# Kernel tuning notes

Hardware: AMD Instinct MI355X
Metric: run time of the kernel (lower is better)

The kernel has to match this reference:

```python
import jax, jax.numpy as jnp
import numpy as np

B = 32768
IN_DIM = 1024
HID = 64
COMM = 256          # comm_dim == proto_latent_dim (num_simultaneous_tokens=1)
K = 8192            # num_protos
BETA = 0.25
KL_WEIGHT = 1.0


def setup_inputs() -> dict:
    key = jax.random.key(0)
    ks = jax.random.split(key, 16)
    def lin(kw, fan_in, shape):
        bound = 1.0 / np.sqrt(fan_in)
        return jax.random.uniform(kw, shape, jnp.float32, -bound, bound)
    return {
        "x": jax.random.normal(ks[0], (B, IN_DIM), jnp.float32),
        "eps": jax.random.normal(ks[1], (B, COMM), jnp.float32),
        "W_feat": lin(ks[2], IN_DIM, (IN_DIM, HID)),
        "b_feat": lin(ks[3], IN_DIM, (HID,)),
        "W0": lin(ks[4], HID, (HID, HID)),
        "b0": lin(ks[5], HID, (HID,)),
        "W1": lin(ks[6], HID, (HID, COMM)),
        "b1": lin(ks[7], HID, (COMM,)),
        "W_mu": lin(ks[8], COMM, (COMM, COMM)),
        "b_mu": lin(ks[9], COMM, (COMM,)),
        "W_var": lin(ks[10], COMM, (COMM, COMM)),
        "b_var": lin(ks[11], COMM, (COMM,)),
        "protos": jax.random.uniform(ks[12], (K, COMM), jnp.float32, -1.0 / K, 1.0 / K),
    }


def reference(x, eps, W_feat, b_feat, W0, b0, W1, b1, W_mu, b_mu, W_var, b_var, protos):
    # feature embedder + MLP (num_layers=2, relu after each)
    h = x @ W_feat + b_feat                       # [B, 64]
    h = jax.nn.relu(h @ W0 + b0)                  # [B, 64]
    h = jax.nn.relu(h @ W1 + b1)                  # [B, 256]
    # variational head
    mu = h @ W_mu + b_mu                          # [B, 256]
    logvar = h @ W_var + b_var                    # [B, 256]
    sample = mu + eps * jnp.exp(0.5 * logvar)     # reparameterize
    # VQ layer: pairwise sq-distances to codebook, argmin, gather
    d = (jnp.sum(sample * sample, axis=1, keepdims=True)
         + jnp.sum(protos * protos, axis=1)
         - 2.0 * (sample @ protos.T))             # [B, K]
    idx = jnp.argmin(d, axis=1)                   # [B]
    q = jnp.take(protos, idx, axis=0)             # [B, 256] == one_hot @ protos
    commitment = jnp.mean((jax.lax.stop_gradient(q) - sample) ** 2)
    embedding = jnp.mean((q - jax.lax.stop_gradient(sample)) ** 2)
    vq_loss = BETA * commitment + embedding
    q_st = sample + jax.lax.stop_gradient(q - sample)  # straight-through
    # KL to standard normal
    kld = jnp.mean(-0.5 * jnp.sum(1.0 + logvar - mu * mu - jnp.exp(logvar), axis=1))
    total_loss = KL_WEIGHT * kld + vq_loss
    return q_st, total_loss, kld
```

## Files before the change

kernel.cpp:

```cpp
#include <hip/hip_runtime.h>
#include <cfloat>

#define B_SZ   32768
#define IN_D   1024
#define HID    64
#define COMM   256
#define NPROTO 8192

#define SSCALE 12.0f
#define PSCALE 1.0e6f

typedef __attribute__((ext_vector_type(8))) short bf16x8;
typedef __attribute__((ext_vector_type(4))) float f32x4;
typedef __attribute__((ext_vector_type(4))) int   i32x4;

#define AS1 __attribute__((address_space(1)))
#define AS3 __attribute__((address_space(3)))

__device__ __forceinline__ unsigned short f2bf(float f) {
    unsigned u = __float_as_uint(f);
    unsigned r = u + 0x7fff + ((u >> 16) & 1);
    return (unsigned short)(r >> 16);
}

__device__ __forceinline__ int f2i8(float f, float scale) {
    float v = fminf(fmaxf(f * scale, -127.f), 127.f);
    return __float2int_rn(v);
}

__global__ __launch_bounds__(256) void prep_weights(
    const float* __restrict__ Wf,  const float* __restrict__ W0,
    const float* __restrict__ W1,  const float* __restrict__ Wmu,
    const float* __restrict__ Wvar,
    unsigned short* __restrict__ Wft, unsigned short* __restrict__ W0t,
    unsigned short* __restrict__ W1t, unsigned short* __restrict__ Wmt,
    unsigned short* __restrict__ Wvt)
{
    int gid = blockIdx.x * 256 + threadIdx.x;
    const float* src; unsigned short* dst; int off, K, N;
    if (gid < 65536)       { src = Wf;  dst = Wft; off = gid;          K = 1024; N = 64;  }
    else if (gid < 69632)  { src = W0;  dst = W0t; off = gid - 65536;  K = 64;   N = 64;  }
    else if (gid < 86016)  { src = W1;  dst = W1t; off = gid - 69632;  K = 64;   N = 256; }
    else if (gid < 151552) { src = Wmu; dst = Wmt; off = gid - 86016;  K = 256;  N = 256; }
    else                   { src = Wvar;dst = Wvt; off = gid - 151552; K = 256;  N = 256; }
    int k = off / N, n = off % N;
    dst[(size_t)n * K + k] = f2bf(src[off]);
}

__global__ __launch_bounds__(256) void pnorm_conv_kernel(const float* __restrict__ protos,
                                                         float* __restrict__ pnormS,
                                                         char* __restrict__ protoq)
{
    int g    = blockIdx.x * 256 + threadIdx.x;
    int p    = g >> 6;
    int lane = g & 63;
    float4 v = *(const float4*)&protos[(size_t)p * COMM + lane * 4];
    int b0 = f2i8(v.x, PSCALE) & 0xff;
    int b1 = f2i8(v.y, PSCALE) & 0xff;
    int b2 = f2i8(v.z, PSCALE) & 0xff;
    int b3 = f2i8(v.w, PSCALE) & 0xff;
    int pk = b0 | (b1 << 8) | (b2 << 16) | (b3 << 24);
    int T = p >> 7, jc = lane >> 2;
    *(int*)(protoq + ((size_t)(T * 16 + jc) * 128 + (p & 127)) * 16 + (lane & 3) * 4) = pk;
    float s = v.x * v.x + v.y * v.y + v.z * v.z + v.w * v.w;
#pragma unroll
    for (int off = 32; off; off >>= 1) s += __shfl_down(s, off);
    if (lane == 0) pnormS[p] = s * (SSCALE * PSCALE);
}

__global__ __launch_bounds__(256) void mlp_fused(
    const float* __restrict__ x,
    const unsigned short* __restrict__ Wft, const float* __restrict__ b_feat,
    const unsigned short* __restrict__ W0t, const float* __restrict__ b0,
    const unsigned short* __restrict__ W1t, const float* __restrict__ b1,
    unsigned short* __restrict__ h3b)
{
    __shared__ __align__(16) char lds[65536];
    short* Xs  = (short*)lds;
    short* Ws  = (short*)(lds + 8192);
    short* H1  = (short*)(lds + 16384);
    short* H2  = (short*)(lds + 24576);
    short* W1s = (short*)(lds + 32768);

    const int t   = threadIdx.x;
    const int w   = t >> 6;
    const int l   = t & 63;
    const int q   = l >> 4;
    const int j16 = l & 15;
    const int rowBase = blockIdx.x * 64;
    const int m = 16 * w + j16;

    float4 xr[2][2];
    int   xp[2];
    auto loadX = [&](int ks) {
#pragma unroll
        for (int i = 0; i < 2; ++i) {
            int p  = i * 256 + t;
            int r  = p >> 3;
            int js = p & 7;
            int j  = js ^ (r & 7);
            const float4* g = (const float4*)(x + (size_t)(rowBase + r) * IN_D + ks * 64 + j * 8);
            xr[i][0] = g[0];
            xr[i][1] = g[1];
            xp[i] = p;
        }
    };

    f32x4 acc1[4];
#pragma unroll
    for (int v = 0; v < 4; ++v) acc1[v] = (f32x4){0.f, 0.f, 0.f, 0.f};

    loadX(0);
    for (int ks = 0; ks < 16; ++ks) {
        __syncthreads();
#pragma unroll
        for (int i = 0; i < 2; ++i) {
            bf16x8 o;
            o[0] = (short)f2bf(xr[i][0].x); o[1] = (short)f2bf(xr[i][0].y);
            o[2] = (short)f2bf(xr[i][0].z); o[3] = (short)f2bf(xr[i][0].w);
            o[4] = (short)f2bf(xr[i][1].x); o[5] = (short)f2bf(xr[i][1].y);
            o[6] = (short)f2bf(xr[i][1].z); o[7] = (short)f2bf(xr[i][1].w);
            *(bf16x8*)((char*)Xs + (size_t)xp[i] * 16) = o;
        }
#pragma unroll
        for (int i = 0; i < 2; ++i) {
            int p  = i * 256 + t;
            int r  = p >> 3;
            int js = p & 7;
            int j  = js ^ (r & 7);
            const unsigned short* gw = Wft + (size_t)r * IN_D + ks * 64 + j * 8;
            void* dw = (char*)Ws + (size_t)(i * 256 + w * 64) * 16;
            __builtin_amdgcn_global_load_lds(
                (const AS1 void*)gw, (AS3 void*)dw, 16, 0, 0);
        }
        if (ks < 15) loadX(ks + 1);
        __syncthreads();
#pragma unroll
        for (int kk = 0; kk < 2; ++kk) {
            int jw = kk * 4 + q;
            bf16x8 af = *(const bf16x8*)((char*)Xs + (size_t)(m * 8 + (jw ^ (m & 7))) * 16);
#pragma unroll
            for (int v = 0; v < 4; ++v) {
                int n = 16 * v + j16;
                bf16x8 bf = *(const bf16x8*)((char*)Ws + (size_t)(n * 8 + (jw ^ (n & 7))) * 16);
                acc1[v] = __builtin_amdgcn_mfma_f32_16x16x32_bf16(af, bf, acc1[v], 0, 0, 0);
            }
        }
    }
#pragma unroll
    for (int v = 0; v < 4; ++v) {
        int c = 16 * v + j16;
        float bb = b_feat[c];
#pragma unroll
        for (int rg = 0; rg < 4; ++rg) {
            int r = 16 * w + q * 4 + rg;
            float h = acc1[v][rg] + bb;
            *(short*)((char*)H1 + (size_t)(r * 8 + ((c >> 3) ^ (r & 7))) * 16 + (c & 7) * 2)
                = (short)f2bf(h);
        }
    }

    __syncthreads();
#pragma unroll
    for (int i = 0; i < 2; ++i) {
        int p  = i * 256 + t;
        int n  = p >> 3;
        int js = p & 7;
        int j  = js ^ (n & 7);
        const unsigned short* gw = W0t + (size_t)n * 64 + j * 8;
        void* dw = (char*)Ws + (size_t)(i * 256 + w * 64) * 16;
        __builtin_amdgcn_global_load_lds(
            (const AS1 void*)gw, (AS3 void*)dw, 16, 0, 0);
    }
    __syncthreads();
    f32x4 acc2[4];
#pragma unroll
    for (int v = 0; v < 4; ++v) acc2[v] = (f32x4){0.f, 0.f, 0.f, 0.f};
#pragma unroll
    for (int kk = 0; kk < 2; ++kk) {
        int jw = kk * 4 + q;
        bf16x8 af = *(const bf16x8*)((char*)H1 + (size_t)(m * 8 + (jw ^ (m & 7))) * 16);
#pragma unroll
        for (int v = 0; v < 4; ++v) {
            int n = 16 * v + j16;
            bf16x8 bf = *(const bf16x8*)((char*)Ws + (size_t)(n * 8 + (jw ^ (n & 7))) * 16);
            acc2[v] = __builtin_amdgcn_mfma_f32_16x16x32_bf16(af, bf, acc2[v], 0, 0, 0);
        }
    }
#pragma unroll
    for (int v = 0; v < 4; ++v) {
        int c = 16 * v + j16;
        float bb = b0[c];
#pragma unroll
        for (int rg = 0; rg < 4; ++rg) {
            int r = 16 * w + q * 4 + rg;
            float h = fmaxf(acc2[v][rg] + bb, 0.f);
            *(short*)((char*)H2 + (size_t)(r * 8 + ((c >> 3) ^ (r & 7))) * 16 + (c & 7) * 2)
                = (short)f2bf(h);
        }
    }

    __syncthreads();
#pragma unroll
    for (int i = 0; i < 8; ++i) {
        int p  = i * 256 + t;
        int n  = p >> 3;
        int js = p & 7;
        int j  = js ^ (n & 7);
        const unsigned short* gw = W1t + (size_t)n * 64 + j * 8;
        void* dw = (char*)W1s + (size_t)(i * 256 + w * 64) * 16;
        __builtin_amdgcn_global_load_lds(
            (const AS1 void*)gw, (AS3 void*)dw, 16, 0, 0);
    }
    __syncthreads();
    f32x4 acc3[16];
#pragma unroll
    for (int v = 0; v < 16; ++v) acc3[v] = (f32x4){0.f, 0.f, 0.f, 0.f};
#pragma unroll
    for (int kk = 0; kk < 2; ++kk) {
        int jw = kk * 4 + q;
        bf16x8 af = *(const bf16x8*)((char*)H2 + (size_t)(m * 8 + (jw ^ (m & 7))) * 16);
#pragma unroll
        for (int v = 0; v < 16; ++v) {
            int n = 16 * v + j16;
            bf16x8 bf = *(const bf16x8*)((char*)W1s + (size_t)(n * 8 + (jw ^ (n & 7))) * 16);
            acc3[v] = __builtin_amdgcn_mfma_f32_16x16x32_bf16(af, bf, acc3[v], 0, 0, 0);
        }
    }
#pragma unroll
    for (int v = 0; v < 16; ++v) {
        int c = 16 * v + j16;
        float bb = b1[c];
#pragma unroll
        for (int rg = 0; rg < 4; ++rg) {
            int row = rowBase + 16 * w + q * 4 + rg;
            float h = fmaxf(acc3[v][rg] + bb, 0.f);
            h3b[(size_t)row * COMM + c] = f2bf(h);
        }
    }
}

__global__ __launch_bounds__(256) void head_mfma(
    const unsigned short* __restrict__ h3b,
    const unsigned short* __restrict__ Wmt, const float* __restrict__ bmu,
    const unsigned short* __restrict__ Wvt, const float* __restrict__ bvar,
    const float* __restrict__ eps,
    float* __restrict__ sample,
    char* __restrict__ sampleq,
    float* __restrict__ klpart)
{
    __shared__ __align__(16) char lds[49152];
    short* H3 = (short*)lds;
    short* Wm = (short*)(lds + 32768);
    short* Wv = (short*)(lds + 40960);

    const int t   = threadIdx.x;
    const int w   = t >> 6;
    const int l   = t & 63;
    const int q   = l >> 4;
    const int j16 = l & 15;
    const int rowBase = blockIdx.x * 64;
    const int m = 16 * w + j16;

#pragma unroll
    for (int i = 0; i < 8; ++i) {
        int p  = i * 256 + t;
        int r  = p >> 5;
        int js = p & 31;
        int j  = (js & 24) | ((js & 7) ^ (r & 7));
        const unsigned short* g = h3b + (size_t)(rowBase + r) * COMM + j * 8;
        void* d = (char*)H3 + (size_t)(i * 256 + w * 64) * 16;
        __builtin_amdgcn_global_load_lds(
            (const AS1 void*)g, (AS3 void*)d, 16, 0, 0);
    }

    float kl = 0.f;
    for (int c = 0; c < 4; ++c) {
        f32x4 am[4], av[4];
#pragma unroll
        for (int v = 0; v < 4; ++v) {
            am[v] = (f32x4){0.f, 0.f, 0.f, 0.f};
            av[v] = (f32x4){0.f, 0.f, 0.f, 0.f};
        }
        for (int ks = 0; ks < 4; ++ks) {
            __syncthreads();
#pragma unroll
            for (int i = 0; i < 2; ++i) {
                int p  = i * 256 + t;
                int n  = p >> 3;
                int js = p & 7;
                int j  = js ^ (n & 7);
                const unsigned short* gm =
                    Wmt + (size_t)(c * 64 + n) * COMM + ks * 64 + j * 8;
                const unsigned short* gv =
                    Wvt + (size_t)(c * 64 + n) * COMM + ks * 64 + j * 8;
                void* dm = (char*)Wm + (size_t)(i * 256 + w * 64) * 16;
                void* dv = (char*)Wv + (size_t)(i * 256 + w * 64) * 16;
                __builtin_amdgcn_global_load_lds(
                    (const AS1 void*)gm, (AS3 void*)dm, 16, 0, 0);
                __builtin_amdgcn_global_load_lds(
                    (const AS1 void*)gv, (AS3 void*)dv, 16, 0, 0);
            }
            __syncthreads();
#pragma unroll
            for (int kk = 0; kk < 2; ++kk) {
                int jwg = ks * 8 + kk * 4 + q;
                bf16x8 af = *(const bf16x8*)((char*)H3 +
                    (size_t)(m * 32 + ((jwg & 24) | ((jwg & 7) ^ (m & 7)))) * 16);
                int jw = kk * 4 + q;
#pragma unroll
                for (int v = 0; v < 4; ++v) {
                    int n = 16 * v + j16;
                    size_t pos = (size_t)(n * 8 + (jw ^ (n & 7))) * 16;
                    bf16x8 bm = *(const bf16x8*)((char*)Wm + pos);
                    bf16x8 bv = *(const bf16x8*)((char*)Wv + pos);
                    am[v] = __builtin_amdgcn_mfma_f32_16x16x32_bf16(af, bm, am[v], 0, 0, 0);
                    av[v] = __builtin_amdgcn_mfma_f32_16x16x32_bf16(af, bv, av[v], 0, 0, 0);
                }
            }
        }
#pragma unroll
        for (int v = 0; v < 4; ++v) {
            int col = c * 64 + 16 * v + j16;
            float bm_ = bmu[col];
            float bv_ = bvar[col];
#pragma unroll
            for (int rg = 0; rg < 4; ++rg) {
                int row = rowBase + 16 * w + q * 4 + rg;
                float mu = am[v][rg] + bm_;
                float lv = av[v][rg] + bv_;
                float e  = expf(0.5f * lv);
                float s  = mu + eps[(size_t)row * COMM + col] * e;
                sample [(size_t)row * COMM + col] = s;
                sampleq[(size_t)row * COMM + col] = (char)f2i8(s, SSCALE);
                kl += 1.f + lv - mu * mu - e * e;
            }
        }
    }
#pragma unroll
    for (int off = 32; off; off >>= 1) kl += __shfl_down(kl, off);
    __shared__ float wsum[4];
    if (l == 0) wsum[w] = kl;
    __syncthreads();
    if (t == 0)
        klpart[blockIdx.x] = wsum[0] + wsum[1] + wsum[2] + wsum[3];
}

#define SPLITS 4
#define SPAN   (NPROTO / SPLITS)
#define NT     (SPAN / 128)

__global__ __launch_bounds__(256) void vq_argmin_i8(
    const char* __restrict__ sampleq,
    const char* __restrict__ protoq,
    const float* __restrict__ pnormS,
    float* __restrict__ minval,
    int* __restrict__ minidx)
{
    __shared__ __align__(16) char As[32768];
    __shared__ __align__(16) char Bs[2][8192];

    const int t   = threadIdx.x;
    const int w   = t >> 6;
    const int l   = t & 63;
    const int q   = l >> 4;
    const int j16 = l & 15;
    const int wrow = (w >> 1) * 64;
    const int wcol = (w & 1) * 64;
    const int rowBase = blockIdx.x * 128;
    const int tBase   = blockIdx.y * NT;

#pragma unroll
    for (int i = 0; i < 8; ++i) {
        int p  = i * 256 + t;
        int r  = p >> 4;
        int cs = p & 15;
        int j  = cs ^ (r & 15);
        const char* g = sampleq + (size_t)(rowBase + r) * COMM + j * 16;
        void* d = As + (size_t)(i * 256 + w * 64) * 16;
        __builtin_amdgcn_global_load_lds(
            (const AS1 void*)g, (AS3 void*)d, 16, 0, 0);
    }
    {
        const char* src = protoq + (size_t)tBase * 32768;
#pragma unroll
        for (int i = 0; i < 2; ++i) {
            int p = i * 256 + t;
            __builtin_amdgcn_global_load_lds(
                (const AS1 void*)(src + (size_t)p * 16),
                (AS3 void*)(Bs[0] + (size_t)(i * 256 + w * 64) * 16), 16, 0, 0);
        }
    }

    float bestv[16];
    int   besti[16];
#pragma unroll
    for (int s = 0; s < 16; ++s) { bestv[s] = FLT_MAX; besti[s] = 0; }

    int buf = 0;
    for (int pt = 0; pt < NT; ++pt) {
        i32x4 acc[4][4];
#pragma unroll
        for (int u = 0; u < 4; ++u)
#pragma unroll
            for (int v = 0; v < 4; ++v) acc[u][v] = (i32x4){0, 0, 0, 0};

        for (int ks = 0; ks < 4; ++ks) {
            __syncthreads();
            int nks = ks + 1, npt = pt;
            if (nks == 4) { nks = 0; ++npt; }
            if (npt < NT) {
                const char* src = protoq + ((size_t)(tBase + npt) * 16 + nks * 4) * 2048;
#pragma unroll
                for (int i = 0; i < 2; ++i) {
                    int p = i * 256 + t;
                    __builtin_amdgcn_global_load_lds(
                        (const AS1 void*)(src + (size_t)p * 16),
                        (AS3 void*)(Bs[buf ^ 1] + (size_t)(i * 256 + w * 64) * 16), 16, 0, 0);
                }
            }
            i32x4 af[4], bfv[4];
            int jc = ks * 4 + q;
#pragma unroll
            for (int u = 0; u < 4; ++u) {
                int mm = wrow + 16 * u + j16;
                af[u] = *(const i32x4*)(As + (size_t)(mm * 16 + (jc ^ (mm & 15))) * 16);
            }
#pragma unroll
            for (int v = 0; v < 4; ++v) {
                int n = wcol + 16 * v + j16;
                bfv[v] = *(const i32x4*)(Bs[buf] + (size_t)(q * 128 + n) * 16);
            }
#pragma unroll
            for (int u = 0; u < 4; ++u)
#pragma unroll
                for (int v = 0; v < 4; ++v)
                    acc[u][v] = __builtin_amdgcn_mfma_i32_16x16x64_i8(
                        af[u], bfv[v], acc[u][v], 0, 0, 0);
            buf ^= 1;
        }
        int pTile = (tBase + pt) * 128;
#pragma unroll
        for (int v = 0; v < 4; ++v) {
            int col  = pTile + wcol + 16 * v + j16;
            float pn = pnormS[col];
#pragma unroll
            for (int u = 0; u < 4; ++u)
#pragma unroll
                for (int rg = 0; rg < 4; ++rg) {
                    float sc   = pn - 2.f * (float)acc[u][v][rg];
                    int   slot = u * 4 + rg;
                    if (sc < bestv[slot]) { bestv[slot] = sc; besti[slot] = col; }
                }
        }
    }
#pragma unroll
    for (int off = 1; off < 16; off <<= 1) {
#pragma unroll
        for (int s = 0; s < 16; ++s) {
            float ov = __shfl_xor(bestv[s], off);
            int   oi = __shfl_xor(besti[s], off);
            if (ov < bestv[s] || (ov == bestv[s] && oi < besti[s])) {
                bestv[s] = ov; besti[s] = oi;
            }
        }
    }
    __syncthreads();
    float* cv = (float*)Bs;
    int*   ci = ((int*)Bs) + 256;
    if (j16 == 0) {
#pragma unroll
        for (int u = 0; u < 4; ++u)
#pragma unroll
            for (int rg = 0; rg < 4; ++rg) {
                int row = wrow + 16 * u + 4 * q + rg;
                cv[(w & 1) * 128 + row] = bestv[u * 4 + rg];
                ci[(w & 1) * 128 + row] = besti[u * 4 + rg];
            }
    }
    __syncthreads();
    if (t < 128) {
        float v0 = cv[t];       int i0 = ci[t];
        float v1 = cv[128 + t]; int i1 = ci[128 + t];
        if (v1 < v0 || (v1 == v0 && i1 < i0)) { v0 = v1; i0 = i1; }
        minval[(size_t)blockIdx.y * B_SZ + rowBase + t] = v0;
        minidx[(size_t)blockIdx.y * B_SZ + rowBase + t] = i0;
    }
}

__global__ __launch_bounds__(256) void gather_kernel(const float* __restrict__ sample,
                                                     const float* __restrict__ protos,
                                                     const float* __restrict__ minval,
                                                     const int* __restrict__ minidx,
                                                     float* __restrict__ out,
                                                     float* __restrict__ msepart)
{
    int t  = threadIdx.x;
    int rb = blockIdx.x * 8;
    __shared__ int sidx[8];
    if (t < 8) {
        int i = rb + t;
        float bv = minval[i];
        int   bi = minidx[i];
#pragma unroll
        for (int s = 1; s < SPLITS; ++s) {
            float v = minval[(size_t)s * B_SZ + i];
            int   j = minidx[(size_t)s * B_SZ + i];
            if (v < bv || (v == bv && j < bi)) { bv = v; bi = j; }
        }
        sidx[t] = bi;
    }
    __syncthreads();
    float part = 0.f;
#pragma unroll
    for (int u = 0; u < 8; ++u) {
        int i  = rb + u;
        int id = sidx[u];
        float qv = protos[(size_t)id * COMM + t];
        float s  = sample[(size_t)i * COMM + t];
        float d  = qv - s;
        out[(size_t)i * COMM + t] = s + d;
        part += d * d;
    }
#pragma unroll
    for (int off = 32; off; off >>= 1) part += __shfl_down(part, off);
    __shared__ float wsum[4];
    if ((t & 63) == 0) wsum[t >> 6] = part;
    __syncthreads();
    if (t == 0) msepart[blockIdx.x] = wsum[0] + wsum[1] + wsum[2] + wsum[3];
}

__global__ __launch_bounds__(256) void finalize_kernel(const float* __restrict__ klpart, int nkl,
                                                       const float* __restrict__ msepart, int nmse,
                                                       float* __restrict__ out)
{
    int t = threadIdx.x;
    double kl = 0.0, mse = 0.0;
    for (int i = t; i < nkl;  i += 256) kl  += (double)klpart[i];
    for (int i = t; i < nmse; i += 256) mse += (double)msepart[i];
#pragma unroll
    for (int off = 32; off; off >>= 1) {
        kl  += __shfl_down(kl, off);
        mse += __shfl_down(mse, off);
    }
    __shared__ double skl[4], smse[4];
    if ((t & 63) == 0) { skl[t >> 6] = kl; smse[t >> 6] = mse; }
    __syncthreads();
    if (t == 0) {
        double K  = skl[0] + skl[1] + skl[2] + skl[3];
        double M  = smse[0] + smse[1] + smse[2] + smse[3];
        double kld = -0.5 * K / (double)B_SZ;
        double vq  = 1.25 * M / ((double)B_SZ * (double)COMM);
        out[(size_t)B_SZ * COMM]     = (float)(kld + vq);
        out[(size_t)B_SZ * COMM + 1] = (float)kld;
    }
}

extern "C" void kernel_launch(void* const* d_in, const int* in_sizes, int n_in,
                              void* d_out, int out_size, void* d_ws, size_t ws_size,
                              hipStream_t stream)
{
    const float* x      = (const float*)d_in[0];
    const float* eps    = (const float*)d_in[1];
    const float* W_feat = (const float*)d_in[2];
    const float* b_feat = (const float*)d_in[3];
    const float* W0     = (const float*)d_in[4];
    const float* b0     = (const float*)d_in[5];
    const float* W1     = (const float*)d_in[6];
    const float* b1     = (const float*)d_in[7];
    const float* W_mu   = (const float*)d_in[8];
    const float* b_mu   = (const float*)d_in[9];
    const float* W_var  = (const float*)d_in[10];
    const float* b_var  = (const float*)d_in[11];
    const float* protos = (const float*)d_in[12];
    float* out = (float*)d_out;

    char* wsb = (char*)d_ws;
    size_t off = 0;
    auto alloc = [&](size_t bytes) -> void* {
        void* p = wsb + off;
        off = (off + bytes + 255) & ~(size_t)255;
        return p;
    };
    unsigned short* Wft     = (unsigned short*)alloc((size_t)IN_D * HID * 2);
    unsigned short* W0t     = (unsigned short*)alloc((size_t)HID * HID * 2);
    unsigned short* W1t     = (unsigned short*)alloc((size_t)HID * COMM * 2);
    unsigned short* Wmt     = (unsigned short*)alloc((size_t)COMM * COMM * 2);
    unsigned short* Wvt     = (unsigned short*)alloc((size_t)COMM * COMM * 2);
    unsigned short* h3b     = (unsigned short*)alloc((size_t)B_SZ * COMM * 2);
    float*          sample  = (float*)alloc((size_t)B_SZ * COMM * 4);
    char*           sampleq = (char*) alloc((size_t)B_SZ * COMM);
    char*           protoq  = (char*) alloc((size_t)NPROTO * COMM);
    float*          pnormS  = (float*)alloc((size_t)NPROTO * 4);
    float*          minval  = (float*)alloc((size_t)SPLITS * B_SZ * 4);
    int*            minidx  = (int*)  alloc((size_t)SPLITS * B_SZ * 4);
    float*          klpart  = (float*)alloc(512 * 4);
    float*          msepart = (float*)alloc(4096 * 4);

    prep_weights<<<848, 256, 0, stream>>>(W_feat, W0, W1, W_mu, W_var,
                                          Wft, W0t, W1t, Wmt, Wvt);
    pnorm_conv_kernel<<<NPROTO / 4, 256, 0, stream>>>(protos, pnormS, protoq);
    mlp_fused<<<B_SZ / 64, 256, 0, stream>>>(x, Wft, b_feat, W0t, b0, W1t, b1, h3b);
    head_mfma<<<B_SZ / 64, 256, 0, stream>>>(h3b, Wmt, b_mu, Wvt, b_var, eps,
                                             sample, sampleq, klpart);
    vq_argmin_i8<<<dim3(B_SZ / 128, SPLITS), 256, 0, stream>>>(sampleq, protoq, pnormS,
                                                               minval, minidx);
    gather_kernel<<<B_SZ / 8, 256, 0, stream>>>(sample, protos, minval, minidx,
                                                out, msepart);
    finalize_kernel<<<1, 256, 0, stream>>>(klpart, 512, msepart, 4096, out);
}
```

Baseline: 428.6 us.

## Merge prep kernels, halve MLP/head row tiles, double-buffer MLP, hoist VQ A-fragments

The two preprocessing kernels are merged into one launch. The MLP and head kernels now use 32-row blocks with a 2x2 wave split, smaller LDS footprints and occupancy hints. The MLP now stages fp32 x straight into LDS with async loads, double-buffers it, and converts to bf16 at fragment load time. The VQ argmin kernel loads all A fragments into registers once instead of on every k-step, and skips the first barrier. The cost is more blocks, duplicated W loads per block, and higher register pressure in the VQ kernel.

```diff
diff --git a/kernel.cpp b/kernel.cpp
--- a/kernel.cpp
+++ b/kernel.cpp
@@ -28,219 +28,217 @@
     return __float2int_rn(v);
 }
 
-__global__ __launch_bounds__(256) void prep_weights(
+__global__ __launch_bounds__(256) void prep_all(
     const float* __restrict__ Wf,  const float* __restrict__ W0,
     const float* __restrict__ W1,  const float* __restrict__ Wmu,
-    const float* __restrict__ Wvar,
+    const float* __restrict__ Wvar, const float* __restrict__ protos,
     unsigned short* __restrict__ Wft, unsigned short* __restrict__ W0t,
     unsigned short* __restrict__ W1t, unsigned short* __restrict__ Wmt,
-    unsigned short* __restrict__ Wvt)
+    unsigned short* __restrict__ Wvt,
+    float* __restrict__ pnormS, char* __restrict__ protoq)
 {
-    int gid = blockIdx.x * 256 + threadIdx.x;
-    const float* src; unsigned short* dst; int off, K, N;
-    if (gid < 65536)       { src = Wf;  dst = Wft; off = gid;          K = 1024; N = 64;  }
-    else if (gid < 69632)  { src = W0;  dst = W0t; off = gid - 65536;  K = 64;   N = 64;  }
-    else if (gid < 86016)  { src = W1;  dst = W1t; off = gid - 69632;  K = 64;   N = 256; }
-    else if (gid < 151552) { src = Wmu; dst = Wmt; off = gid - 86016;  K = 256;  N = 256; }
-    else                   { src = Wvar;dst = Wvt; off = gid - 151552; K = 256;  N = 256; }
-    int k = off / N, n = off % N;
-    dst[(size_t)n * K + k] = f2bf(src[off]);
-}
-
-__global__ __launch_bounds__(256) void pnorm_conv_kernel(const float* __restrict__ protos,
-                                                         float* __restrict__ pnormS,
-                                                         char* __restrict__ protoq)
-{
-    int g    = blockIdx.x * 256 + threadIdx.x;
-    int p    = g >> 6;
-    int lane = g & 63;
-    float4 v = *(const float4*)&protos[(size_t)p * COMM + lane * 4];
-    int b0 = f2i8(v.x, PSCALE) & 0xff;
-    int b1 = f2i8(v.y, PSCALE) & 0xff;
-    int b2 = f2i8(v.z, PSCALE) & 0xff;
-    int b3 = f2i8(v.w, PSCALE) & 0xff;
-    int pk = b0 | (b1 << 8) | (b2 << 16) | (b3 << 24);
-    int T = p >> 7, jc = lane >> 2;
-    *(int*)(protoq + ((size_t)(T * 16 + jc) * 128 + (p & 127)) * 16 + (lane & 3) * 4) = pk;
-    float s = v.x * v.x + v.y * v.y + v.z * v.z + v.w * v.w;
-#pragma unroll
-    for (int off = 32; off; off >>= 1) s += __shfl_down(s, off);
-    if (lane == 0) pnormS[p] = s * (SSCALE * PSCALE);
-}
-
-__global__ __launch_bounds__(256) void mlp_fused(
+    int bid = blockIdx.x;
+    if (bid < 848) {
+        int gid = bid * 256 + threadIdx.x;
+        const float* src; unsigned short* dst; int off, K, N;
+        if (gid < 65536)       { src = Wf;  dst = Wft; off = gid;          K = 1024; N = 64;  }
+        else if (gid < 69632)  { src = W0;  dst = W0t; off = gid - 65536;  K = 64;   N = 64;  }
+        else if (gid < 86016)  { src = W1;  dst = W1t; off = gid - 69632;  K = 64;   N = 256; }
+        else if (gid < 151552) { src = Wmu; dst = Wmt; off = gid - 86016;  K = 256;  N = 256; }
+        else                   { src = Wvar;dst = Wvt; off = gid - 151552; K = 256;  N = 256; }
+        int k = off / N, n = off % N;
+        dst[(size_t)n * K + k] = f2bf(src[off]);
+    } else {
+        int g    = (bid - 848) * 256 + threadIdx.x;
+        int p    = g >> 6;
+        int lane = g & 63;
+        float4 v = *(const float4*)&protos[(size_t)p * COMM + lane * 4];
+        int b0 = f2i8(v.x, PSCALE) & 0xff;
+        int b1 = f2i8(v.y, PSCALE) & 0xff;
+        int b2 = f2i8(v.z, PSCALE) & 0xff;
+        int b3 = f2i8(v.w, PSCALE) & 0xff;
+        int pk = b0 | (b1 << 8) | (b2 << 16) | (b3 << 24);
+        int T = p >> 7, jc = lane >> 2;
+        *(int*)(protoq + ((size_t)(T * 16 + jc) * 128 + (p & 127)) * 16 + (lane & 3) * 4) = pk;
+        float s = v.x * v.x + v.y * v.y + v.z * v.z + v.w * v.w;
+#pragma unroll
+        for (int off = 32; off; off >>= 1) s += __shfl_down(s, off);
+        if (lane == 0) pnormS[p] = s * (SSCALE * PSCALE);
+    }
+}
+
+__global__ __launch_bounds__(256, 4) void mlp_fused(
     const float* __restrict__ x,
     const unsigned short* __restrict__ Wft, const float* __restrict__ b_feat,
     const unsigned short* __restrict__ W0t, const float* __restrict__ b0,
     const unsigned short* __restrict__ W1t, const float* __restrict__ b1,
     unsigned short* __restrict__ h3b)
 {
-    __shared__ __align__(16) char lds[65536];
-    short* Xs  = (short*)lds;
-    short* Ws  = (short*)(lds + 8192);
-    short* H1  = (short*)(lds + 16384);
-    short* H2  = (short*)(lds + 24576);
-    short* W1s = (short*)(lds + 32768);
+    __shared__ __align__(16) char lds[40960];
+    char* Xs0 = lds;
+    char* Xs1 = lds + 8192;
+    char* Ws0 = lds + 16384;
+    char* Ws1 = lds + 24576;
+    char* H1  = lds + 32768;
+    char* H2  = lds + 36864;
 
     const int t   = threadIdx.x;
     const int w   = t >> 6;
     const int l   = t & 63;
     const int q   = l >> 4;
     const int j16 = l & 15;
-    const int rowBase = blockIdx.x * 64;
-    const int m = 16 * w + j16;
-
-    float4 xr[2][2];
-    int   xp[2];
-    auto loadX = [&](int ks) {
+    const int rh  = w >> 1;
+    const int ch  = w & 1;
+    const int rowBase = blockIdx.x * 32;
+    const int m = rh * 16 + j16;
+
+    auto stageX = [&](int ks, char* dst) {
 #pragma unroll
         for (int i = 0; i < 2; ++i) {
             int p  = i * 256 + t;
-            int r  = p >> 3;
-            int js = p & 7;
-            int j  = js ^ (r & 7);
-            const float4* g = (const float4*)(x + (size_t)(rowBase + r) * IN_D + ks * 64 + j * 8);
-            xr[i][0] = g[0];
-            xr[i][1] = g[1];
-            xp[i] = p;
+            int r  = p >> 4;
+            int cs = p & 15;
+            int j  = cs ^ (r & 15);
+            const float* g = x + (size_t)(rowBase + r) * IN_D + ks * 64 + j * 4;
+            void* d = dst + (size_t)(i * 256 + w * 64) * 16;
+            __builtin_amdgcn_global_load_lds((const AS1 void*)g, (AS3 void*)d, 16, 0, 0);
         }
     };
-
-    f32x4 acc1[4];
-#pragma unroll
-    for (int v = 0; v < 4; ++v) acc1[v] = (f32x4){0.f, 0.f, 0.f, 0.f};
-
-    loadX(0);
-    for (int ks = 0; ks < 16; ++ks) {
-        __syncthreads();
-#pragma unroll
-        for (int i = 0; i < 2; ++i) {
-            bf16x8 o;
-            o[0] = (short)f2bf(xr[i][0].x); o[1] = (short)f2bf(xr[i][0].y);
-            o[2] = (short)f2bf(xr[i][0].z); o[3] = (short)f2bf(xr[i][0].w);
-            o[4] = (short)f2bf(xr[i][1].x); o[5] = (short)f2bf(xr[i][1].y);
-            o[6] = (short)f2bf(xr[i][1].z); o[7] = (short)f2bf(xr[i][1].w);
-            *(bf16x8*)((char*)Xs + (size_t)xp[i] * 16) = o;
-        }
+    auto stageW = [&](const unsigned short* Wt, int ldk, int ks, char* dst) {
 #pragma unroll
         for (int i = 0; i < 2; ++i) {
             int p  = i * 256 + t;
-            int r  = p >> 3;
-            int js = p & 7;
-            int j  = js ^ (r & 7);
-            const unsigned short* gw = Wft + (size_t)r * IN_D + ks * 64 + j * 8;
-            void* dw = (char*)Ws + (size_t)(i * 256 + w * 64) * 16;
-            __builtin_amdgcn_global_load_lds(
-                (const AS1 void*)gw, (AS3 void*)dw, 16, 0, 0);
-        }
-        if (ks < 15) loadX(ks + 1);
+            int n  = p >> 3;
+            int cs = p & 7;
+            int j  = cs ^ (n & 7);
+            const unsigned short* g = Wt + (size_t)n * ldk + ks * 64 + j * 8;
+            void* d = dst + (size_t)(i * 256 + w * 64) * 16;
+            __builtin_amdgcn_global_load_lds((const AS1 void*)g, (AS3 void*)d, 16, 0, 0);
+        }
+    };
+    auto afragX = [&](const char* Xsb, int kk) -> bf16x8 {
+        int jc = kk * 8 + q * 2;
+        f32x4 a0 = *(const f32x4*)(Xsb + (size_t)(m * 16 + (jc ^ (m & 15))) * 16);
+        f32x4 a1 = *(const f32x4*)(Xsb + (size_t)(m * 16 + ((jc + 1) ^ (m & 15))) * 16);
+        bf16x8 o;
+        o[0] = (short)f2bf(a0[0]); o[1] = (short)f2bf(a0[1]);
+        o[2] = (short)f2bf(a0[2]); o[3] = (short)f2bf(a0[3]);
+        o[4] = (short)f2bf(a1[0]); o[5] = (short)f2bf(a1[1]);
+        o[6] = (short)f2bf(a1[2]); o[7] = (short)f2bf(a1[3]);
+        return o;
+    };
+    auto bfrag = [&](const char* Wsb, int kk, int v) -> bf16x8 {
+        int n  = ch * 32 + 16 * v + j16;
+        int jc = kk * 4 + q;
+        return *(const bf16x8*)(Wsb + (size_t)(n * 8 + (jc ^ (n & 7))) * 16);
+    };
+    auto afragH = [&](const char* Hs, int kk) -> bf16x8 {
+        int jc = kk * 4 + q;
+        return *(const bf16x8*)(Hs + (size_t)(m * 8 + (jc ^ (m & 7))) * 16);
+    };
+
+    f32x4 acc1[2];
+#pragma unroll
+    for (int v = 0; v < 2; ++v) acc1[v] = (f32x4){0.f, 0.f, 0.f, 0.f};
+
+    stageX(0, Xs0);
+    stageW(Wft, IN_D, 0, Ws0);
+    for (int ks = 0; ks < 16; ++ks) {
+        int buf = ks & 1;
         __syncthreads();
+        if (ks < 15) {
+            stageX(ks + 1, buf ? Xs0 : Xs1);
+            stageW(Wft, IN_D, ks + 1, buf ? Ws0 : Ws1);
+        }
+        const char* Xsb = buf ? Xs1 : Xs0;
+        const char* Wsb = buf ? Ws1 : Ws0;
 #pragma unroll
         for (int kk = 0; kk < 2; ++kk) {
-            int jw = kk * 4 + q;
-            bf16x8 af = *(const bf16x8*)((char*)Xs + (size_t)(m * 8 + (jw ^ (m & 7))) * 16);
-#pragma unroll
-            for (int v = 0; v < 4; ++v) {
-                int n = 16 * v + j16;
-                bf16x8 bf = *(const bf16x8*)((char*)Ws + (size_t)(n * 8 + (jw ^ (n & 7))) * 16);
-                acc1[v] = __builtin_amdgcn_mfma_f32_16x16x32_bf16(af, bf, acc1[v], 0, 0, 0);
-            }
-        }
-    }
-#pragma unroll
-    for (int v = 0; v < 4; ++v) {
-        int c = 16 * v + j16;
+            bf16x8 af = afragX(Xsb, kk);
+#pragma unroll
+            for (int v = 0; v < 2; ++v)
+                acc1[v] = __builtin_amdgcn_mfma_f32_16x16x32_bf16(
+                    af, bfrag(Wsb, kk, v), acc1[v], 0, 0, 0);
+        }
+    }
+#pragma unroll
+    for (int v = 0; v < 2; ++v) {
+        int c = ch * 32 + 16 * v + j16;
         float bb = b_feat[c];
 #pragma unroll
         for (int rg = 0; rg < 4; ++rg) {
-            int r = 16 * w + q * 4 + rg;
+            int r = rh * 16 + q * 4 + rg;
             float h = acc1[v][rg] + bb;
-            *(short*)((char*)H1 + (size_t)(r * 8 + ((c >> 3) ^ (r & 7))) * 16 + (c & 7) * 2)
+            *(short*)(H1 + (size_t)(r * 8 + ((c >> 3) ^ (r & 7))) * 16 + (c & 7) * 2)
                 = (short)f2bf(h);
         }
     }
-
-    __syncthreads();
-#pragma unroll
-    for (int i = 0; i < 2; ++i) {
-        int p  = i * 256 + t;
-        int n  = p >> 3;
-        int js = p & 7;
-        int j  = js ^ (n & 7);
-        const unsigned short* gw = W0t + (size_t)n * 64 + j * 8;
-        void* dw = (char*)Ws + (size_t)(i * 256 + w * 64) * 16;
-        __builtin_amdgcn_global_load_lds(
-            (const AS1 void*)gw, (AS3 void*)dw, 16, 0, 0);
-    }
-    __syncthreads();
-    f32x4 acc2[4];
-#pragma unroll
-    for (int v = 0; v < 4; ++v) acc2[v] = (f32x4){0.f, 0.f, 0.f, 0.f};
+    stageW(W0t, 64, 0, Ws0);
+    __syncthreads();
+
+    f32x4 acc2[2];
+#pragma unroll
+    for (int v = 0; v < 2; ++v) acc2[v] = (f32x4){0.f, 0.f, 0.f, 0.f};
 #pragma unroll
     for (int kk = 0; kk < 2; ++kk) {
-        int jw = kk * 4 + q;
-        bf16x8 af = *(const bf16x8*)((char*)H1 + (size_t)(m * 8 + (jw ^ (m & 7))) * 16);
-#pragma unroll
-        for (int v = 0; v < 4; ++v) {
-            int n = 16 * v + j16;
-            bf16x8 bf = *(const bf16x8*)((char*)Ws + (size_t)(n * 8 + (jw ^ (n & 7))) * 16);
-            acc2[v] = __builtin_amdgcn_mfma_f32_16x16x32_bf16(af, bf, acc2[v], 0, 0, 0);
-        }
-    }
-#pragma unroll
-    for (int v = 0; v < 4; ++v) {
-        int c = 16 * v + j16;
+        bf16x8 af = afragH(H1, kk);
+#pragma unroll
+        for (int v = 0; v < 2; ++v)
+            acc2[v] = __builtin_amdgcn_mfma_f32_16x16x32_bf16(
+                af, bfrag(Ws0, kk, v), acc2[v], 0, 0, 0);
+    }
+#pragma unroll
+    for (int v = 0; v < 2; ++v) {
+        int c = ch * 32 + 16 * v + j16;
         float bb = b0[c];
 #pragma unroll
         for (int rg = 0; rg < 4; ++rg) {
-            int r = 16 * w + q * 4 + rg;
+            int r = rh * 16 + q * 4 + rg;
             float h = fmaxf(acc2[v][rg] + bb, 0.f);
-            *(short*)((char*)H2 + (size_t)(r * 8 + ((c >> 3) ^ (r & 7))) * 16 + (c & 7) * 2)
+            *(short*)(H2 + (size_t)(r * 8 + ((c >> 3) ^ (r & 7))) * 16 + (c & 7) * 2)
                 = (short)f2bf(h);
         }
     }
-
-    __syncthreads();
-#pragma unroll
-    for (int i = 0; i < 8; ++i) {
-        int p  = i * 256 + t;
-        int n  = p >> 3;
-        int js = p & 7;
-        int j  = js ^ (n & 7);
-        const unsigned short* gw = W1t + (size_t)n * 64 + j * 8;
-        void* dw = (char*)W1s + (size_t)(i * 256 + w * 64) * 16;
-        __builtin_amdgcn_global_load_lds(
-            (const AS1 void*)gw, (AS3 void*)dw, 16, 0, 0);
-    }
-    __syncthreads();
-    f32x4 acc3[16];
-#pragma unroll
-    for (int v = 0; v < 16; ++v) acc3[v] = (f32x4){0.f, 0.f, 0.f, 0.f};
-#pragma unroll
-    for (int kk = 0; kk < 2; ++kk) {
-        int jw = kk * 4 + q;
-        bf16x8 af = *(const bf16x8*)((char*)H2 + (size_t)(m * 8 + (jw ^ (m & 7))) * 16);
-#pragma unroll
-        for (int v = 0; v < 16; ++v) {
-            int n = 16 * v + j16;
-            bf16x8 bf = *(const bf16x8*)((char*)W1s + (size_t)(n * 8 + (jw ^ (n & 7))) * 16);
-            acc3[v] = __builtin_amdgcn_mfma_f32_16x16x32_bf16(af, bf, acc3[v], 0, 0, 0);
-        }
-    }
-#pragma unroll
-    for (int v = 0; v < 16; ++v) {
-        int c = 16 * v + j16;
-        float bb = b1[c];
-#pragma unroll
-        for (int rg = 0; rg < 4; ++rg) {
-            int row = rowBase + 16 * w + q * 4 + rg;
-            float h = fmaxf(acc3[v][rg] + bb, 0.f);
-            h3b[(size_t)row * COMM + c] = f2bf(h);
-        }
-    }
-}
-
-__global__ __launch_bounds__(256) void head_mfma(
+    stageW(W1t, 64, 0, Ws1);
+    __syncthreads();
+
+    auto stage3 = [&](int c4, const char* Wsb) {
+        f32x4 acc[2];
+#pragma unroll
+        for (int v = 0; v < 2; ++v) acc[v] = (f32x4){0.f, 0.f, 0.f, 0.f};
+#pragma unroll
+        for (int kk = 0; kk < 2; ++kk) {
+            bf16x8 af = afragH(H2, kk);
+#pragma unroll
+            for (int v = 0; v < 2; ++v)
+                acc[v] = __builtin_amdgcn_mfma_f32_16x16x32_bf16(
+                    af, bfrag(Wsb, kk, v), acc[v], 0, 0, 0);
+        }
+#pragma unroll
+        for (int v = 0; v < 2; ++v) {
+            int col = c4 * 64 + ch * 32 + 16 * v + j16;
+            float bb = b1[col];
+#pragma unroll
+            for (int rg = 0; rg < 4; ++rg) {
+                int row = rowBase + rh * 16 + q * 4 + rg;
+                float h = fmaxf(acc[v][rg] + bb, 0.f);
+                h3b[(size_t)row * COMM + col] = f2bf(h);
+            }
+        }
+    };
+    stageW(W1t + (size_t)64 * 64, 64, 0, Ws0);
+    stage3(0, Ws1);
+    __syncthreads();
+    stageW(W1t + (size_t)128 * 64, 64, 0, Ws1);
+    stage3(1, Ws0);
+    __syncthreads();
+    stageW(W1t + (size_t)192 * 64, 64, 0, Ws0);
+    stage3(2, Ws1);
+    __syncthreads();
+    stage3(3, Ws0);
+}
+
+__global__ __launch_bounds__(256, 4) void head_mfma(
     const unsigned short* __restrict__ h3b,
     const unsigned short* __restrict__ Wmt, const float* __restrict__ bmu,
     const unsigned short* __restrict__ Wvt, const float* __restrict__ bvar,
@@ -249,36 +247,37 @@
     char* __restrict__ sampleq,
     float* __restrict__ klpart)
 {
-    __shared__ __align__(16) char lds[49152];
-    short* H3 = (short*)lds;
-    short* Wm = (short*)(lds + 32768);
-    short* Wv = (short*)(lds + 40960);
+    __shared__ __align__(16) char lds[32768];
+    char* H3 = lds;
+    char* Wm = lds + 16384;
+    char* Wv = lds + 24576;
 
     const int t   = threadIdx.x;
     const int w   = t >> 6;
     const int l   = t & 63;
     const int q   = l >> 4;
     const int j16 = l & 15;
-    const int rowBase = blockIdx.x * 64;
-    const int m = 16 * w + j16;
-
-#pragma unroll
-    for (int i = 0; i < 8; ++i) {
+    const int rh  = w >> 1;
+    const int ch  = w & 1;
+    const int rowBase = blockIdx.x * 32;
+    const int m = rh * 16 + j16;
+
+#pragma unroll
+    for (int i = 0; i < 4; ++i) {
         int p  = i * 256 + t;
         int r  = p >> 5;
         int js = p & 31;
         int j  = (js & 24) | ((js & 7) ^ (r & 7));
         const unsigned short* g = h3b + (size_t)(rowBase + r) * COMM + j * 8;
-        void* d = (char*)H3 + (size_t)(i * 256 + w * 64) * 16;
-        __builtin_amdgcn_global_load_lds(
-            (const AS1 void*)g, (AS3 void*)d, 16, 0, 0);
+        void* d = H3 + (size_t)(i * 256 + w * 64) * 16;
+        __builtin_amdgcn_global_load_lds((const AS1 void*)g, (AS3 void*)d, 16, 0, 0);
     }
 
     float kl = 0.f;
     for (int c = 0; c < 4; ++c) {
-        f32x4 am[4], av[4];
-#pragma unroll
-        for (int v = 0; v < 4; ++v) {
+        f32x4 am[2], av[2];
+#pragma unroll
+        for (int v = 0; v < 2; ++v) {
             am[v] = (f32x4){0.f, 0.f, 0.f, 0.f};
             av[v] = (f32x4){0.f, 0.f, 0.f, 0.f};
         }
@@ -294,39 +293,37 @@
                     Wmt + (size_t)(c * 64 + n) * COMM + ks * 64 + j * 8;
                 const unsigned short* gv =
                     Wvt + (size_t)(c * 64 + n) * COMM + ks * 64 + j * 8;
-                void* dm = (char*)Wm + (size_t)(i * 256 + w * 64) * 16;
-                void* dv = (char*)Wv + (size_t)(i * 256 + w * 64) * 16;
-                __builtin_amdgcn_global_load_lds(
-                    (const AS1 void*)gm, (AS3 void*)dm, 16, 0, 0);
-                __builtin_amdgcn_global_load_lds(
-                    (const AS1 void*)gv, (AS3 void*)dv, 16, 0, 0);
+                void* dm = Wm + (size_t)(i * 256 + w * 64) * 16;
+                void* dv = Wv + (size_t)(i * 256 + w * 64) * 16;
+                __builtin_amdgcn_global_load_lds((const AS1 void*)gm, (AS3 void*)dm, 16, 0, 0);
+                __builtin_amdgcn_global_load_lds((const AS1 void*)gv, (AS3 void*)dv, 16, 0, 0);
             }
             __syncthreads();
 #pragma unroll
             for (int kk = 0; kk < 2; ++kk) {
                 int jwg = ks * 8 + kk * 4 + q;
-                bf16x8 af = *(const bf16x8*)((char*)H3 +
+                bf16x8 af = *(const bf16x8*)(H3 +
                     (size_t)(m * 32 + ((jwg & 24) | ((jwg & 7) ^ (m & 7)))) * 16);
                 int jw = kk * 4 + q;
 #pragma unroll
-                for (int v = 0; v < 4; ++v) {
-                    int n = 16 * v + j16;
+                for (int v = 0; v < 2; ++v) {
+                    int n = ch * 32 + 16 * v + j16;
                     size_t pos = (size_t)(n * 8 + (jw ^ (n & 7))) * 16;
-                    bf16x8 bm = *(const bf16x8*)((char*)Wm + pos);
-                    bf16x8 bv = *(const bf16x8*)((char*)Wv + pos);
+                    bf16x8 bm = *(const bf16x8*)(Wm + pos);
+                    bf16x8 bv = *(const bf16x8*)(Wv + pos);
                     am[v] = __builtin_amdgcn_mfma_f32_16x16x32_bf16(af, bm, am[v], 0, 0, 0);
                     av[v] = __builtin_amdgcn_mfma_f32_16x16x32_bf16(af, bv, av[v], 0, 0, 0);
                 }
             }
         }
 #pragma unroll
-        for (int v = 0; v < 4; ++v) {
-            int col = c * 64 + 16 * v + j16;
+        for (int v = 0; v < 2; ++v) {
+            int col = c * 64 + ch * 32 + 16 * v + j16;
             float bm_ = bmu[col];
             float bv_ = bvar[col];
 #pragma unroll
             for (int rg = 0; rg < 4; ++rg) {
-                int row = rowBase + 16 * w + q * 4 + rg;
+                int row = rowBase + rh * 16 + q * 4 + rg;
                 float mu = am[v][rg] + bm_;
                 float lv = av[v][rg] + bv_;
                 float e  = expf(0.5f * lv);
@@ -350,7 +347,7 @@
 #define SPAN   (NPROTO / SPLITS)
 #define NT     (SPAN / 128)
 
-__global__ __launch_bounds__(256) void vq_argmin_i8(
+__global__ __launch_bounds__(256, 2) void vq_argmin_i8(
     const char* __restrict__ sampleq,
     const char* __restrict__ protoq,
     const float* __restrict__ pnormS,
@@ -378,8 +375,7 @@
         int j  = cs ^ (r & 15);
         const char* g = sampleq + (size_t)(rowBase + r) * COMM + j * 16;
         void* d = As + (size_t)(i * 256 + w * 64) * 16;
-        __builtin_amdgcn_global_load_lds(
-            (const AS1 void*)g, (AS3 void*)d, 16, 0, 0);
+        __builtin_amdgcn_global_load_lds((const AS1 void*)g, (AS3 void*)d, 16, 0, 0);
     }
     {
         const char* src = protoq + (size_t)tBase * 32768;
@@ -391,6 +387,17 @@
                 (AS3 void*)(Bs[0] + (size_t)(i * 256 + w * 64) * 16), 16, 0, 0);
         }
     }
+    __syncthreads();
+
+    i32x4 af[4][4];
+#pragma unroll
+    for (int u = 0; u < 4; ++u)
+#pragma unroll
+        for (int ks = 0; ks < 4; ++ks) {
+            int mm = wrow + 16 * u + j16;
+            int jc = ks * 4 + q;
+            af[u][ks] = *(const i32x4*)(As + (size_t)(mm * 16 + (jc ^ (mm & 15))) * 16);
+        }
 
     float bestv[16];
     int   besti[16];
@@ -406,7 +413,7 @@
             for (int v = 0; v < 4; ++v) acc[u][v] = (i32x4){0, 0, 0, 0};
 
         for (int ks = 0; ks < 4; ++ks) {
-            __syncthreads();
+            if (pt | ks) __syncthreads();
             int nks = ks + 1, npt = pt;
             if (nks == 4) { nks = 0; ++npt; }
             if (npt < NT) {
@@ -419,13 +426,7 @@
                         (AS3 void*)(Bs[buf ^ 1] + (size_t)(i * 256 + w * 64) * 16), 16, 0, 0);
                 }
             }
-            i32x4 af[4], bfv[4];
-            int jc = ks * 4 + q;
-#pragma unroll
-            for (int u = 0; u < 4; ++u) {
-                int mm = wrow + 16 * u + j16;
-                af[u] = *(const i32x4*)(As + (size_t)(mm * 16 + (jc ^ (mm & 15))) * 16);
-            }
+            i32x4 bfv[4];
 #pragma unroll
             for (int v = 0; v < 4; ++v) {
                 int n = wcol + 16 * v + j16;
@@ -436,7 +437,7 @@
 #pragma unroll
                 for (int v = 0; v < 4; ++v)
                     acc[u][v] = __builtin_amdgcn_mfma_i32_16x16x64_i8(
-                        af[u], bfv[v], acc[u][v], 0, 0, 0);
+                        af[u][ks], bfv[v], acc[u][v], 0, 0, 0);
             buf ^= 1;
         }
         int pTile = (tBase + pt) * 128;
@@ -594,18 +595,17 @@
     float*          pnormS  = (float*)alloc((size_t)NPROTO * 4);
     float*          minval  = (float*)alloc((size_t)SPLITS * B_SZ * 4);
     int*            minidx  = (int*)  alloc((size_t)SPLITS * B_SZ * 4);
-    float*          klpart  = (float*)alloc(512 * 4);
+    float*          klpart  = (float*)alloc(1024 * 4);
     float*          msepart = (float*)alloc(4096 * 4);
 
-    prep_weights<<<848, 256, 0, stream>>>(W_feat, W0, W1, W_mu, W_var,
-                                          Wft, W0t, W1t, Wmt, Wvt);
-    pnorm_conv_kernel<<<NPROTO / 4, 256, 0, stream>>>(protos, pnormS, protoq);
-    mlp_fused<<<B_SZ / 64, 256, 0, stream>>>(x, Wft, b_feat, W0t, b0, W1t, b1, h3b);
-    head_mfma<<<B_SZ / 64, 256, 0, stream>>>(h3b, Wmt, b_mu, Wvt, b_var, eps,
+    prep_all<<<2896, 256, 0, stream>>>(W_feat, W0, W1, W_mu, W_var, protos,
+                                       Wft, W0t, W1t, Wmt, Wvt, pnormS, protoq);
+    mlp_fused<<<B_SZ / 32, 256, 0, stream>>>(x, Wft, b_feat, W0t, b0, W1t, b1, h3b);
+    head_mfma<<<B_SZ / 32, 256, 0, stream>>>(h3b, Wmt, b_mu, Wvt, b_var, eps,
                                              sample, sampleq, klpart);
     vq_argmin_i8<<<dim3(B_SZ / 128, SPLITS), 256, 0, stream>>>(sampleq, protoq, pnormS,
                                                                minval, minidx);
     gather_kernel<<<B_SZ / 8, 256, 0, stream>>>(sample, protos, minval, minidx,
                                                 out, msepart);
-    finalize_kernel<<<1, 256, 0, stream>>>(klpart, 512, msepart, 4096, out);
-}
+    finalize_kernel<<<1, 256, 0, stream>>>(klpart, 1024, msepart, 4096, out);
+}
```

New measurement: 419.1 us. -2.2%, faster.
